# Optimization experiments

Measured on AMD Instinct MI355X. Metric: run time of the kernel, lower is better.

The kernel has to match this reference:

```python
import jax, jax.numpy as jnp
import numpy as np

D_MODEL = 3072
N_HEADS = 24
HEAD_DIM = D_MODEL // N_HEADS          # 128
Q_PROJ = D_MODEL // 2                  # 1536
KV_PROJ = 2 * D_MODEL // 3             # 2048
ROPE_DIM = HEAD_DIM // 2               # 64 (qk_rope_dim == qk_no_rope_dim)
MAX_LEN = 2048
ROPE_THETA = 10000.0
EPS = 1e-6
B, S = 2, 2048


def setup_inputs() -> dict:
    key = jax.random.key(0)
    ks = jax.random.split(key, 7)
    return {
        "x": jax.random.normal(ks[0], (B, S, D_MODEL), dtype=jnp.float32),
        "scale": jnp.ones((D_MODEL,), dtype=jnp.float32),
        "w_dq": 0.01 * jax.random.normal(ks[1], (D_MODEL, Q_PROJ), dtype=jnp.float32),
        "w_uq": 0.01 * jax.random.normal(ks[2], (Q_PROJ, D_MODEL), dtype=jnp.float32),
        "w_dkv": 0.01 * jax.random.normal(ks[3], (D_MODEL, KV_PROJ + ROPE_DIM), dtype=jnp.float32),
        "w_ukv": 0.01 * jax.random.normal(ks[4], (KV_PROJ, D_MODEL + N_HEADS * ROPE_DIM), dtype=jnp.float32),
        "w_o": 0.01 * jax.random.normal(ks[5], (D_MODEL, D_MODEL), dtype=jnp.float32),
    }


def _rope_cos_sin(seq_len):
    # freqs over full head_dim, sliced to rope_dim//2 then tiled x2 (as in torch repeat)
    freqs = 1.0 / (ROPE_THETA ** (jnp.arange(0, HEAD_DIM, 2, dtype=jnp.float32) / HEAD_DIM))
    angles = jnp.arange(seq_len, dtype=jnp.float32)[:, None] * freqs[None, :]  # [S, 64]
    ang = angles[:, : ROPE_DIM // 2]                                            # [S, 32]
    cos = jnp.tile(jnp.cos(ang), (1, 2))                                        # [S, 64]
    sin = jnp.tile(jnp.sin(ang), (1, 2))
    return cos[None, None], sin[None, None]  # [1,1,S,64]


def _rotate_half(t):
    a, b = jnp.split(t, 2, axis=-1)
    return jnp.concatenate([-b, a], axis=-1)


def reference(x, scale, w_dq, w_uq, w_dkv, w_ukv, w_o):
    b, s, _ = x.shape
    # RMSNorm pre-normalization
    xn = scale * (x * jax.lax.rsqrt(jnp.mean(x * x, axis=-1, keepdims=True) + EPS))
    # two-stage query projection
    q = (xn @ w_dq) @ w_uq                                   # [B,S,D]
    q = q.reshape(b, s, N_HEADS, HEAD_DIM).transpose(0, 2, 1, 3)  # [B,H,S,hd]
    q_no_rope, q_rope = jnp.split(q, [ROPE_DIM], axis=-1)
    cos, sin = _rope_cos_sin(s)
    q_rope = q_rope * cos + _rotate_half(q_rope) * sin
    # KV down projection (this is the kv cache)
    kv_down = xn @ w_dkv                                     # [B,S,KV_PROJ+rope]
    kv_no_rope, k_rope = jnp.split(kv_down, [KV_PROJ], axis=-1)
    # KV up projection
    kv_up = kv_no_rope @ w_ukv                               # [B,S,H*(hd+rope)]
    kv_up = kv_up.reshape(b, s, N_HEADS, HEAD_DIM + ROPE_DIM).transpose(0, 2, 1, 3)
    key, value = jnp.split(kv_up, [ROPE_DIM], axis=-1)       # key [B,H,S,64], value [B,H,S,128]
    # shared rope key (one head, broadcast to all heads)
    k_rope = k_rope[:, None, :, :]                           # [B,1,S,64]
    k_rope = k_rope * cos + _rotate_half(k_rope) * sin
    k_rope = jnp.broadcast_to(k_rope, (b, N_HEADS, s, ROPE_DIM))
    final_q = jnp.concatenate([q_no_rope, q_rope], axis=-1)  # [B,H,S,128]
    final_k = jnp.concatenate([key, k_rope], axis=-1)        # [B,H,S,128]
    # masked SDPA (causal, past_length=0)
    inv_scale = 1.0 / jnp.sqrt(jnp.asarray(HEAD_DIM, dtype=x.dtype))
    scores = jnp.einsum("bhsd,bhtd->bhst", final_q, final_k) * inv_scale
    causal = jnp.tril(jnp.ones((s, s), dtype=bool))
    scores = jnp.where(causal[None, None], scores, jnp.asarray(-1e30, dtype=scores.dtype))
    attn = jax.nn.softmax(scores, axis=-1)
    attn_out = jnp.einsum("bhst,bhtd->bhsd", attn, value)    # [B,H,S,128]
    attn_out = attn_out.transpose(0, 2, 1, 3).reshape(b, s, D_MODEL)
    output = attn_out @ w_o.T
    return output, kv_down
```

## Files before the change

### kernel.cpp

```cpp
#include <hip/hip_runtime.h>
#include <hip/hip_bf16.h>
#include <stdint.h>

using bf16_t = __bf16;
using bf16x8 = __attribute__((ext_vector_type(8))) __bf16;
using bf16x4 = __attribute__((ext_vector_type(4))) __bf16;
using f32x4  = __attribute__((ext_vector_type(4))) float;

#define D_MODEL 3072
#define N_HEADS 24
#define HEAD_DIM 128
#define Q_PROJ 1536
#define KV_PROJ 2048
#define ROPE_DIM 64
#define S_LEN 2048
#define NTOK 4096
#define KVDN 2112
#define KVUN 4608

__device__ __forceinline__ void async_ld16(const void* g, void* l) {
    __builtin_amdgcn_global_load_lds(
        (__attribute__((address_space(1))) uint32_t*)(uintptr_t)g,
        (__attribute__((address_space(3))) uint32_t*)(uint32_t)(uintptr_t)l,
        16, 0, 0);
}

#define BARRIER() __builtin_amdgcn_s_barrier()
#define WAITVN(n) asm volatile("s_waitcnt vmcnt(" #n ")" ::: "memory")

__global__ __launch_bounds__(256) void rmsnorm_kernel(
    const float* __restrict__ x, const float* __restrict__ sc, bf16_t* __restrict__ xn)
{
    const int tok = blockIdx.x;
    const int t = threadIdx.x;
    const float4* xr = (const float4*)(x + (size_t)tok * D_MODEL);
    float4 a = xr[t], b = xr[t + 256], c = xr[t + 512];
    float ss = a.x*a.x + a.y*a.y + a.z*a.z + a.w*a.w
             + b.x*b.x + b.y*b.y + b.z*b.z + b.w*b.w
             + c.x*c.x + c.y*c.y + c.z*c.z + c.w*c.w;
    #pragma unroll
    for (int off = 32; off >= 1; off >>= 1) ss += __shfl_xor(ss, off);
    __shared__ float red[4];
    if ((t & 63) == 0) red[t >> 6] = ss;
    __syncthreads();
    const float inv = rsqrtf((red[0] + red[1] + red[2] + red[3]) * (1.0f / D_MODEL) + 1e-6f);
    const float4* sr = (const float4*)sc;
    float4 s0 = sr[t], s1 = sr[t + 256], s2 = sr[t + 512];
    bf16x4* xo = (bf16x4*)(xn + (size_t)tok * D_MODEL);
    bf16x4 o;
    o[0]=(bf16_t)(a.x*s0.x*inv); o[1]=(bf16_t)(a.y*s0.y*inv); o[2]=(bf16_t)(a.z*s0.z*inv); o[3]=(bf16_t)(a.w*s0.w*inv);
    xo[t] = o;
    o[0]=(bf16_t)(b.x*s1.x*inv); o[1]=(bf16_t)(b.y*s1.y*inv); o[2]=(bf16_t)(b.z*s1.z*inv); o[3]=(bf16_t)(b.w*s1.w*inv);
    xo[t + 256] = o;
    o[0]=(bf16_t)(c.x*s2.x*inv); o[1]=(bf16_t)(c.y*s2.y*inv); o[2]=(bf16_t)(c.z*s2.z*inv); o[3]=(bf16_t)(c.w*s2.w*inv);
    xo[t + 512] = o;
}

__global__ __launch_bounds__(256) void prep_weights(
    const float* __restrict__ w_dq, const float* __restrict__ w_uq,
    const float* __restrict__ w_dkv, const float* __restrict__ w_ukv,
    const float* __restrict__ w_o,
    bf16_t* __restrict__ wcat, bf16_t* __restrict__ wuqt,
    bf16_t* __restrict__ wukvt, bf16_t* __restrict__ wob)
{
    __shared__ float tile[32][33];
    int t = blockIdx.x;
    const float* in; bf16_t* out; int K, N, ntx; bool tr = true;
    if (t < 4608)        {            in = w_dq;  out = wcat;                          K = 3072; N = 1536; ntx = 48; }
    else if (t < 10944)  { t -= 4608; in = w_dkv; out = wcat + (size_t)1536 * 3072;    K = 3072; N = 2112; ntx = 66; }
    else if (t < 15552)  { t -= 10944; in = w_uq;  out = wuqt;                         K = 1536; N = 3072; ntx = 96; }
    else if (t < 24768)  { t -= 15552; in = w_ukv; out = wukvt;                        K = 2048; N = 4608; ntx = 144; }
    else                 { t -= 24768; in = w_o;   out = wob;                          K = 3072; N = 3072; ntx = 96; tr = false; }
    const int n0 = (t % ntx) * 32, k0 = (t / ntx) * 32;
    const int tx = threadIdx.x, ty = threadIdx.y;
    if (tr) {
        #pragma unroll
        for (int i = 0; i < 32; i += 8)
            tile[ty + i][tx] = in[(size_t)(k0 + ty + i) * N + n0 + tx];
        __syncthreads();
        #pragma unroll
        for (int i = 0; i < 32; i += 8)
            out[(size_t)(n0 + ty + i) * K + k0 + tx] = (bf16_t)tile[tx][ty + i];
    } else {
        #pragma unroll
        for (int i = 0; i < 32; i += 8)
            out[(size_t)(k0 + ty + i) * N + n0 + tx] =
                (bf16_t)in[(size_t)(k0 + ty + i) * N + n0 + tx];
    }
}

template<int RH, int BNF>
__device__ __forceinline__ void mfmaQ(f32x4 (&acc)[8][BNF], const bf16x8 (&af)[4],
                                      const bf16x8 (&bfv)[BNF]) {
    __builtin_amdgcn_s_setprio(1);
    #pragma unroll
    for (int i = 0; i < 4; ++i)
        #pragma unroll
        for (int cf = 0; cf < BNF; ++cf)
            acc[RH*4+i][cf] = __builtin_amdgcn_mfma_f32_16x16x32_bf16(af[i], bfv[cf], acc[RH*4+i][cf], 0, 0, 0);
    __builtin_amdgcn_s_setprio(0);
}

template<int BNF>
__global__ __launch_bounds__(512, 2) void gemm256(
    const bf16_t* __restrict__ A, const bf16_t* __restrict__ B, int N, int K,
    float* __restrict__ Cf, int ldf, int flo, int fhi,
    bf16_t* __restrict__ Cb1, int ldb1, int b1lo, int b1hi,
    bf16_t* __restrict__ Cb2, int ldb2, int b2lo, int b2hi,
    bf16_t* __restrict__ vt, float cbscale)
{
    constexpr int BN = BNF * 64;
    constexpr uint32_t BSLOT = BNF * 4096;
    __shared__ char LDS[65536 + 4 * BSLOT];
    char* Lc = LDS;
    const int tid = threadIdx.x;
    const int wv = tid >> 6, lane = tid & 63;
    const int fr = lane & 15, fg = lane >> 4;
    const int wr = wv >> 2, wc = wv & 3;
    const bool bwave = (wv < 2 * BNF);

    int lin = blockIdx.y * gridDim.x + blockIdx.x;
    const int nwg = gridDim.x * gridDim.y;
    if ((nwg & 7) == 0) lin = (lin & 7) * (nwg >> 3) + (lin >> 3);
    const int bx = lin % gridDim.x, by = lin / gridDim.x;
    const int m0 = by << 8, n0 = bx * BN;

    const uint32_t slot4 = (uint32_t)((fg ^ ((fr >> 1) & 3)) << 4);

    const bf16_t* agp[2]; const bf16_t* bgp[2];
    uint32_t aoff[2], boff[2];
    #pragma unroll
    for (int j = 0; j < 2; ++j) {
        const int c = j * 512 + tid;
        const int g = c ^ ((c >> 3) & 3);
        agp[j] = A + (size_t)(m0 + (g >> 2)) * K + (g & 3) * 8;
        aoff[j] = (uint32_t)((j * 8 + wv) * 1024);
        const int cb = j * (BNF * 128) + tid;
        const int gb = cb ^ ((cb >> 3) & 3);
        int br = n0 + (gb >> 2); if (br > N - 1) br = N - 1;
        bgp[j] = B + (size_t)br * K + (gb & 3) * 8;
        boff[j] = (uint32_t)(j * (BNF * 2048) + wv * 1024);
    }

    f32x4 acc[8][BNF];
    f32x4 zero = {0.f, 0.f, 0.f, 0.f};
    #pragma unroll
    for (int i = 0; i < 8; ++i)
        #pragma unroll
        for (int j = 0; j < BNF; ++j) acc[i][j] = zero;

    bf16x8 A0[4], A1[4], B0[BNF], B1[BNF];
    const int rowA = (wr << 7) + fr;
    const int rowB = wc * (BNF * 16) + fr;

    auto stA = [&](int t, int kh) {
        const uint32_t sb = (uint32_t)(((2*t + kh) & 3) << 14);
        #pragma unroll
        for (int j = 0; j < 2; ++j)
            async_ld16(agp[j] + t * 64 + kh * 32, Lc + sb + aoff[j]);
    };
    auto stB = [&](int t, int kh) {
        const uint32_t sb = 65536u + (uint32_t)(((2*t + kh) & 3) * BSLOT);
        if (tid < BNF * 128) {
            #pragma unroll
            for (int j = 0; j < 2; ++j)
                async_ld16(bgp[j] + t * 64 + kh * 32, Lc + sb + boff[j]);
        }
    };
    auto ldA4 = [&](int t, int kh, int rh, bf16x8 (&dst)[4]) {
        const uint32_t base = (uint32_t)(((2*t + kh) & 3) << 14);
        #pragma unroll
        for (int i = 0; i < 4; ++i)
            dst[i] = *(const bf16x8*)(Lc + base + (rowA + (rh * 4 + i) * 16) * 64 + slot4);
    };
    auto ldBn = [&](int t, int kh, bf16x8 (&dst)[BNF]) {
        const uint32_t base = 65536u + (uint32_t)(((2*t + kh) & 3) * BSLOT);
        #pragma unroll
        for (int cf = 0; cf < BNF; ++cf)
            dst[cf] = *(const bf16x8*)(Lc + base + (rowB + cf * 16) * 64 + slot4);
    };

    const int NT = K >> 6;
    stA(0, 0); stB(0, 0); stA(0, 1); stB(0, 1);
    stA(1, 0); stB(1, 0); stA(1, 1); stB(1, 1);
    if (bwave) { WAITVN(8); } else { WAITVN(4); }
    BARRIER();
    ldA4(0, 0, 0, A0); ldBn(0, 0, B0);

    for (int t = 0; t < NT; ++t) {
        const bool pref = (t + 2 < NT);
        ldA4(t, 0, 1, A1);
        mfmaQ<0, BNF>(acc, A0, B0);
        if (pref) { if (bwave) { WAITVN(4); } else { WAITVN(2); } }
        else      { WAITVN(0); }
        BARRIER();
        ldA4(t, 1, 0, A0); ldBn(t, 1, B1);
        if (pref) { stA(t + 2, 0); stB(t + 2, 0); }
        mfmaQ<1, BNF>(acc, A1, B0);
        BARRIER();
        ldA4(t, 1, 1, A1);
        mfmaQ<0, BNF>(acc, A0, B1);
        BARRIER();
        if (t + 1 < NT) { ldA4(t + 1, 0, 0, A0); ldBn(t + 1, 0, B0); }
        if (pref) { stA(t + 2, 1); stB(t + 2, 1); }
        mfmaQ<1, BNF>(acc, A1, B1);
        BARRIER();
    }

    const int colb = n0 + wc * (BNF * 16) + fr;
    const int rowb = m0 + (wr << 7) + fg * 4;
    if (vt) {
        #pragma unroll
        for (int rf = 0; rf < 8; ++rf) {
            const int row0 = rowb + rf * 16;
            const int bb = row0 >> 11, s0 = row0 & 2047;
            #pragma unroll
            for (int cf = 0; cf < BNF; ++cf) {
                const int col = colb + cf * 16;
                const int h = col / 192;
                const int dm = col - h * 192;
                if (dm < 64) {
                    #pragma unroll
                    for (int r = 0; r < 4; ++r)
                        Cb1[(size_t)(row0 + r) * ldb1 + col] = (bf16_t)acc[rf][cf][r];
                } else {
                    bf16x4 o;
                    o[0] = (bf16_t)acc[rf][cf][0];
                    o[1] = (bf16_t)acc[rf][cf][1];
                    o[2] = (bf16_t)acc[rf][cf][2];
                    o[3] = (bf16_t)acc[rf][cf][3];
                    *(bf16x4*)(vt + ((size_t)((bb * 24 + h) * 128 + dm - 64)) * 2048 + s0) = o;
                }
            }
        }
    } else {
        #pragma unroll
        for (int rf = 0; rf < 8; ++rf)
            #pragma unroll
            for (int cf = 0; cf < BNF; ++cf) {
                const int col = colb + cf * 16;
                #pragma unroll
                for (int r = 0; r < 4; ++r) {
                    const int row = rowb + rf * 16 + r;
                    const float v = acc[rf][cf][r];
                    if (Cf  && col >= flo  && col < fhi)  Cf [(size_t)row * ldf  + col - flo]  = v;
                    if (Cb1 && col >= b1lo && col < b1hi) Cb1[(size_t)row * ldb1 + col - b1lo] = (bf16_t)(v * cbscale);
                    if (Cb2 && col >= b2lo && col < b2hi) Cb2[(size_t)row * ldb2 + col - b2lo] = (bf16_t)v;
                }
            }
    }
}

__global__ void rope_tab(float* __restrict__ ctab, float* __restrict__ stab)
{
    const int idx = blockIdx.x * 256 + threadIdx.x;
    if (idx >= S_LEN * 32) return;
    const int s = idx >> 5, i = idx & 31;
    const float freq = powf(10000.0f, -(float)(2 * i) * (1.0f / 128.0f));
    const float ang = (float)s * freq;
    ctab[idx] = cosf(ang);
    stab[idx] = sinf(ang);
}

__global__ __launch_bounds__(256) void rope_all(
    bf16_t* __restrict__ q, const float* __restrict__ kvd, bf16_t* __restrict__ kr,
    const float* __restrict__ ctab, const float* __restrict__ stab)
{
    const int idx = blockIdx.x * 256 + threadIdx.x;
    if (idx < NTOK * N_HEADS * 4) {
        const int c = idx & 3;
        const int rest = idx >> 2;
        const int h = rest % N_HEADS;
        const int tok = rest / N_HEADS;
        const int s = tok & (S_LEN - 1);
        bf16_t* p = q + (size_t)tok * D_MODEL + h * HEAD_DIM + 64 + c * 8;
        bf16x8 a = *(const bf16x8*)(p);
        bf16x8 b = *(const bf16x8*)(p + 32);
        const float4* cp = (const float4*)(ctab + s * 32 + c * 8);
        const float4* sp = (const float4*)(stab + s * 32 + c * 8);
        float4 c0 = cp[0], c1 = cp[1];
        float4 s0 = sp[0], s1 = sp[1];
        float cs[8] = {c0.x, c0.y, c0.z, c0.w, c1.x, c1.y, c1.z, c1.w};
        float sn[8] = {s0.x, s0.y, s0.z, s0.w, s1.x, s1.y, s1.z, s1.w};
        bf16x8 oa, ob;
        #pragma unroll
        for (int j = 0; j < 8; ++j) {
            const float av = (float)a[j], bv = (float)b[j];
            oa[j] = (bf16_t)(av * cs[j] - bv * sn[j]);
            ob[j] = (bf16_t)(bv * cs[j] + av * sn[j]);
        }
        *(bf16x8*)(p)      = oa;
        *(bf16x8*)(p + 32) = ob;
    } else {
        const int kx = idx - NTOK * N_HEADS * 4;
        if (kx >= NTOK * 32) return;
        const int i = kx & 31;
        const int tok = kx >> 5;
        const int s = tok & (S_LEN - 1);
        const float* p = kvd + (size_t)tok * KVDN + KV_PROJ;
        const float a = p[i], b = p[i + 32];
        const float c = ctab[s * 32 + i], sn = stab[s * 32 + i];
        kr[(size_t)tok * 64 + i]      = (bf16_t)(a * c - b * sn);
        kr[(size_t)tok * 64 + i + 32] = (bf16_t)(b * c + a * sn);
    }
}

__global__ __launch_bounds__(256, 2) void attn_fwd(
    const bf16_t* __restrict__ Q, const bf16_t* __restrict__ KVUP,
    const bf16_t* __restrict__ KR, const bf16_t* __restrict__ VT,
    bf16_t* __restrict__ AO)
{
    __shared__ bf16_t Knr[2][64 * 64];
    __shared__ bf16_t Krp[2][64 * 64];
    __shared__ bf16_t Vls[2][128 * 64];

    const int bh = blockIdx.y;
    const int b = bh / N_HEADS, h = bh % N_HEADS;
    const int wave = threadIdx.x >> 6, lane = threadIdx.x & 63;
    const int fr = lane & 15, fg = lane >> 4;
    const int rx = fr & 7;
    const int hi = fg >> 1;
    const int s0l = fr + 32 * (fg & 1);
    const int s1l = s0l + 16;

    const bf16_t* Kb  = KVUP + (size_t)b * S_LEN * KVUN + (size_t)h * 192;
    const bf16_t* KRb = KR + (size_t)b * S_LEN * 64;
    const bf16_t* Vb  = VT + (size_t)bh * HEAD_DIM * S_LEN;

    const int srow   = lane >> 3;
    const int schunk = (lane & 7) ^ srow;

    f32x4 zero = {0.f, 0.f, 0.f, 0.f};

    #pragma unroll 1
    for (int tp = 0; tp < 2; ++tp) {
        const int qt = (tp == 0) ? blockIdx.x : (15 - blockIdx.x);
        const int qb = qt * 128;
        const int wrow0 = qb + wave * 32;

        bf16x8 qf[2][4];
        #pragma unroll
        for (int rf = 0; rf < 2; ++rf)
            #pragma unroll
            for (int kc = 0; kc < 4; ++kc)
                qf[rf][kc] = *(const bf16x8*)(Q + (size_t)(b * S_LEN + wrow0 + rf * 16 + fr) * D_MODEL
                                              + h * HEAD_DIM + kc * 32 + fg * 8);
        f32x4 oacc[2][8];
        float m_i[2], l_i[2];
        #pragma unroll
        for (int rf = 0; rf < 2; ++rf) {
            #pragma unroll
            for (int nf = 0; nf < 8; ++nf) oacc[rf][nf] = zero;
            m_i[rf] = -1e30f; l_i[rf] = 0.f;
        }

        auto stage = [&](int kvb, int bf) {
            #pragma unroll
            for (int c = 0; c < 2; ++c) {
                const int r0 = wave * 16 + c * 8;
                async_ld16(Kb  + (size_t)(kvb + r0 + srow) * KVUN + schunk * 8, &Knr[bf][r0 * 64]);
                async_ld16(KRb + (size_t)(kvb + r0 + srow) * 64   + schunk * 8, &Krp[bf][r0 * 64]);
            }
            #pragma unroll
            for (int c = 0; c < 4; ++c) {
                const int r0 = wave * 32 + c * 8;
                async_ld16(Vb + (size_t)(r0 + srow) * S_LEN + kvb + schunk * 8, &Vls[bf][r0 * 64]);
            }
        };

        const int kvend = qb + 128;
        int cur = 0;
        stage(0, 0);
        __syncthreads();

        #pragma unroll 1
        for (int kvb = 0; kvb < kvend; kvb += 64) {
            if (kvb + 64 < kvend) stage(kvb + 64, cur ^ 1);

            if (kvb <= wrow0 + 31) {
                const bf16_t* Kc = Knr[cur];
                const bf16_t* Rc = Krp[cur];
                const bf16_t* Vc = Vls[cur];

                f32x4 sacc[2][4];
                #pragma unroll
                for (int rf = 0; rf < 2; ++rf)
                    #pragma unroll
                    for (int jn = 0; jn < 4; ++jn) sacc[rf][jn] = zero;
                __builtin_amdgcn_s_setprio(1);
                #pragma unroll
                for (int jn = 0; jn < 4; ++jn) {
                    const int krow = jn * 16 + fr;
                    bf16x8 kA = *(const bf16x8*)(Kc + krow * 64 + (((0 + fg) ^ rx) << 3));
                    bf16x8 kB = *(const bf16x8*)(Kc + krow * 64 + (((4 + fg) ^ rx) << 3));
                    bf16x8 kC = *(const bf16x8*)(Rc + krow * 64 + (((0 + fg) ^ rx) << 3));
                    bf16x8 kD = *(const bf16x8*)(Rc + krow * 64 + (((4 + fg) ^ rx) << 3));
                    #pragma unroll
                    for (int rf = 0; rf < 2; ++rf) {
                        sacc[rf][jn] = __builtin_amdgcn_mfma_f32_16x16x32_bf16(kA, qf[rf][0], sacc[rf][jn], 0, 0, 0);
                        sacc[rf][jn] = __builtin_amdgcn_mfma_f32_16x16x32_bf16(kB, qf[rf][1], sacc[rf][jn], 0, 0, 0);
                        sacc[rf][jn] = __builtin_amdgcn_mfma_f32_16x16x32_bf16(kC, qf[rf][2], sacc[rf][jn], 0, 0, 0);
                        sacc[rf][jn] = __builtin_amdgcn_mfma_f32_16x16x32_bf16(kD, qf[rf][3], sacc[rf][jn], 0, 0, 0);
                    }
                }
                __builtin_amdgcn_s_setprio(0);

                const bool needMask = (kvb + 63 > wrow0);
                uint32_t pk[2][4][2];
                #pragma unroll
                for (int rf = 0; rf < 2; ++rf) {
                    const int qrow = wrow0 + rf * 16 + fr;
                    float mx = -1e30f;
                    #pragma unroll
                    for (int jn = 0; jn < 4; ++jn)
                        #pragma unroll
                        for (int r = 0; r < 4; ++r) {
                            float v = sacc[rf][jn][r];
                            if (needMask && (kvb + jn * 16 + fg * 4 + r > qrow)) v = -1e30f;
                            sacc[rf][jn][r] = v;
                            mx = fmaxf(mx, v);
                        }
                    mx = fmaxf(mx, __shfl_xor(mx, 16));
                    mx = fmaxf(mx, __shfl_xor(mx, 32));
                    if (!__all(mx <= m_i[rf] + 8.f)) {
                        const float mn = fmaxf(m_i[rf], mx);
                        const float sc = __builtin_amdgcn_exp2f(m_i[rf] - mn);
                        m_i[rf] = mn;
                        l_i[rf] *= sc;
                        #pragma unroll
                        for (int nf = 0; nf < 8; ++nf)
                            #pragma unroll
                            for (int r = 0; r < 4; ++r) oacc[rf][nf][r] *= sc;
                    }
                    const float mn = m_i[rf];
                    float ls = 0.f;
                    #pragma unroll
                    for (int jn = 0; jn < 4; ++jn) {
                        float p0 = __builtin_amdgcn_exp2f(sacc[rf][jn][0] - mn);
                        float p1 = __builtin_amdgcn_exp2f(sacc[rf][jn][1] - mn);
                        float p2 = __builtin_amdgcn_exp2f(sacc[rf][jn][2] - mn);
                        float p3 = __builtin_amdgcn_exp2f(sacc[rf][jn][3] - mn);
                        ls += (p0 + p1) + (p2 + p3);
                        union { bf16x4 h; uint32_t w[2]; } cv;
                        cv.h[0] = (bf16_t)p0; cv.h[1] = (bf16_t)p1;
                        cv.h[2] = (bf16_t)p2; cv.h[3] = (bf16_t)p3;
                        pk[rf][jn][0] = cv.w[0]; pk[rf][jn][1] = cv.w[1];
                    }
                    ls += __shfl_xor(ls, 16);
                    ls += __shfl_xor(ls, 32);
                    l_i[rf] += ls;
                }

                bf16x8 bfr[2][2];
                #pragma unroll
                for (int rf = 0; rf < 2; ++rf)
                    #pragma unroll
                    for (int ks = 0; ks < 2; ++ks) {
                        const uint32_t t00 = __shfl(pk[rf][2*ks][0],   s0l);
                        const uint32_t t01 = __shfl(pk[rf][2*ks][1],   s0l);
                        const uint32_t t10 = __shfl(pk[rf][2*ks+1][0], s0l);
                        const uint32_t t11 = __shfl(pk[rf][2*ks+1][1], s0l);
                        const uint32_t u00 = __shfl(pk[rf][2*ks][0],   s1l);
                        const uint32_t u01 = __shfl(pk[rf][2*ks][1],   s1l);
                        const uint32_t u10 = __shfl(pk[rf][2*ks+1][0], s1l);
                        const uint32_t u11 = __shfl(pk[rf][2*ks+1][1], s1l);
                        union { bf16x8 h; uint32_t w[4]; } bb;
                        bb.w[0] = hi ? t10 : t00;
                        bb.w[1] = hi ? t11 : t01;
                        bb.w[2] = hi ? u10 : u00;
                        bb.w[3] = hi ? u11 : u01;
                        bfr[rf][ks] = bb.h;
                    }

                __builtin_amdgcn_s_setprio(1);
                #pragma unroll
                for (int nf = 0; nf < 8; ++nf) {
                    const int vrow = nf * 16 + fr;
                    bf16x8 v0 = *(const bf16x8*)(Vc + vrow * 64 + (((0 + fg) ^ rx) << 3));
                    bf16x8 v1 = *(const bf16x8*)(Vc + vrow * 64 + (((4 + fg) ^ rx) << 3));
                    #pragma unroll
                    for (int rf = 0; rf < 2; ++rf) {
                        oacc[rf][nf] = __builtin_amdgcn_mfma_f32_16x16x32_bf16(v0, bfr[rf][0], oacc[rf][nf], 0, 0, 0);
                        oacc[rf][nf] = __builtin_amdgcn_mfma_f32_16x16x32_bf16(v1, bfr[rf][1], oacc[rf][nf], 0, 0, 0);
                    }
                }
                __builtin_amdgcn_s_setprio(0);
            }
            __syncthreads();
            cur ^= 1;
        }

        #pragma unroll
        for (int rf = 0; rf < 2; ++rf) {
            const float rl = __builtin_amdgcn_rcpf(l_i[rf]);
            const int qrow = wrow0 + rf * 16 + fr;
            bf16_t* aob = AO + (size_t)(b * S_LEN + qrow) * D_MODEL + h * HEAD_DIM + fg * 4;
            #pragma unroll
            for (int nf = 0; nf < 8; ++nf) {
                bf16x4 o;
                o[0] = (bf16_t)(oacc[rf][nf][0] * rl);
                o[1] = (bf16_t)(oacc[rf][nf][1] * rl);
                o[2] = (bf16_t)(oacc[rf][nf][2] * rl);
                o[3] = (bf16_t)(oacc[rf][nf][3] * rl);
                *(bf16x4*)(aob + nf * 16) = o;
            }
        }
    }
}

extern "C" void kernel_launch(void* const* d_in, const int* in_sizes, int n_in,
                              void* d_out, int out_size, void* d_ws, size_t ws_size,
                              hipStream_t stream)
{
    const float* x     = (const float*)d_in[0];
    const float* scale = (const float*)d_in[1];
    const float* w_dq  = (const float*)d_in[2];
    const float* w_uq  = (const float*)d_in[3];
    const float* w_dkv = (const float*)d_in[4];
    const float* w_ukv = (const float*)d_in[5];
    const float* w_o   = (const float*)d_in[6];
    float* out0 = (float*)d_out;
    float* out1 = out0 + (size_t)NTOK * D_MODEL;

    if (ws_size < 187039744ull) return;
    char* ws = (char*)d_ws;
    bf16_t* XN    = (bf16_t*)(ws + 0);
    bf16_t* WCAT  = (bf16_t*)(ws + 25165824ull);
    bf16_t* WUQT  = (bf16_t*)(ws + 47579136ull);
    bf16_t* WUKVT = (bf16_t*)(ws + 57016320ull);
    bf16_t* WOB   = (bf16_t*)(ws + 75890688ull);
    bf16_t* QD    = (bf16_t*)(ws + 94765056ull);
    bf16_t* Qb    = (bf16_t*)(ws + 107347968ull);
    bf16_t* KVNR  = (bf16_t*)(ws + 132513792ull);
    bf16_t* KVUP  = (bf16_t*)(ws + 149291008ull);
    bf16_t* KRB   = (bf16_t*)(ws + 94765056ull);
    float*  CTAB  = (float*) (ws + 95289344ull);
    float*  STAB  = (float*) (ws + 95551488ull);
    bf16_t* VTb   = WCAT;
    bf16_t* AO    = XN;

    const float l2e_isc = 0.127500625f;

    rmsnorm_kernel<<<NTOK, 256, 0, stream>>>(x, scale, XN);
    prep_weights<<<33984, dim3(32, 8), 0, stream>>>(w_dq, w_uq, w_dkv, w_ukv, w_o,
                                                    WCAT, WUQT, WUKVT, WOB);

    gemm256<4><<<dim3(15, 16), 512, 0, stream>>>(XN, WCAT, 3648, 3072,
        out1, KVDN, 1536, 3648,
        QD,   Q_PROJ, 0, 1536,
        KVNR, KV_PROJ, 1536, 3584, nullptr, 1.0f);
    gemm256<3><<<dim3(16, 16), 512, 0, stream>>>(QD, WUQT, 3072, 1536,
        nullptr, 0, 0, 0, Qb, D_MODEL, 0, 3072, nullptr, 0, 0, 0, nullptr, l2e_isc);
    rope_tab<<<(S_LEN * 32 + 255) / 256, 256, 0, stream>>>(CTAB, STAB);
    rope_all<<<2048, 256, 0, stream>>>(Qb, out1, KRB, CTAB, STAB);
    gemm256<3><<<dim3(24, 16), 512, 0, stream>>>(KVNR, WUKVT, 4608, 2048,
        nullptr, 0, 0, 0, KVUP, KVUN, 0, 0, nullptr, 0, 0, 0, VTb, 1.0f);
    attn_fwd<<<dim3(8, 48), 256, 0, stream>>>(Qb, KVUP, KRB, VTb, AO);
    gemm256<3><<<dim3(16, 16), 512, 0, stream>>>(AO, WOB, 3072, 3072,
        out0, D_MODEL, 0, 3072, nullptr, 0, 0, 0, nullptr, 0, 0, 0, nullptr, 1.0f);
}
```

Measured before the change: 505.2 us.

## Add 128x192-tile GEMM kernel for up-projection and output GEMMs, vectorize w_o conversion

Adds a gemm128 kernel with 128x192 output tiles, smaller LDS and four blocks per CU, and uses it for the Q up-projection, KV up-projection and output projection. gemm256 keeps only the fused down-projection. Smaller tiles double the grid (256 blocks become 512, 384 become 768), so these GEMMs fill the 256 CUs more evenly and lose less to tail waves. The cost is lower per-tile data reuse and more global traffic. The w_o fp32-to-bf16 copy in prep_weights also moves to a flat float4 path.

```diff
diff --git a/kernel.cpp b/kernel.cpp
--- a/kernel.cpp
+++ b/kernel.cpp
@@ -65,28 +65,29 @@
 {
     __shared__ float tile[32][33];
     int t = blockIdx.x;
-    const float* in; bf16_t* out; int K, N, ntx; bool tr = true;
+    if (t >= 24768) {
+        const int tt = t - 24768;
+        const int idx = tt * 256 + threadIdx.y * 32 + threadIdx.x;
+        float4 v = ((const float4*)w_o)[idx];
+        bf16x4 o;
+        o[0] = (bf16_t)v.x; o[1] = (bf16_t)v.y; o[2] = (bf16_t)v.z; o[3] = (bf16_t)v.w;
+        ((bf16x4*)wob)[idx] = o;
+        return;
+    }
+    const float* in; bf16_t* out; int K, N, ntx;
     if (t < 4608)        {            in = w_dq;  out = wcat;                          K = 3072; N = 1536; ntx = 48; }
     else if (t < 10944)  { t -= 4608; in = w_dkv; out = wcat + (size_t)1536 * 3072;    K = 3072; N = 2112; ntx = 66; }
     else if (t < 15552)  { t -= 10944; in = w_uq;  out = wuqt;                         K = 1536; N = 3072; ntx = 96; }
-    else if (t < 24768)  { t -= 15552; in = w_ukv; out = wukvt;                        K = 2048; N = 4608; ntx = 144; }
-    else                 { t -= 24768; in = w_o;   out = wob;                          K = 3072; N = 3072; ntx = 96; tr = false; }
+    else                 { t -= 15552; in = w_ukv; out = wukvt;                        K = 2048; N = 4608; ntx = 144; }
     const int n0 = (t % ntx) * 32, k0 = (t / ntx) * 32;
     const int tx = threadIdx.x, ty = threadIdx.y;
-    if (tr) {
-        #pragma unroll
-        for (int i = 0; i < 32; i += 8)
-            tile[ty + i][tx] = in[(size_t)(k0 + ty + i) * N + n0 + tx];
-        __syncthreads();
-        #pragma unroll
-        for (int i = 0; i < 32; i += 8)
-            out[(size_t)(n0 + ty + i) * K + k0 + tx] = (bf16_t)tile[tx][ty + i];
-    } else {
-        #pragma unroll
-        for (int i = 0; i < 32; i += 8)
-            out[(size_t)(k0 + ty + i) * N + n0 + tx] =
-                (bf16_t)in[(size_t)(k0 + ty + i) * N + n0 + tx];
-    }
+    #pragma unroll
+    for (int i = 0; i < 32; i += 8)
+        tile[ty + i][tx] = in[(size_t)(k0 + ty + i) * N + n0 + tx];
+    __syncthreads();
+    #pragma unroll
+    for (int i = 0; i < 32; i += 8)
+        out[(size_t)(n0 + ty + i) * K + k0 + tx] = (bf16_t)tile[tx][ty + i];
 }
 
 template<int RH, int BNF>
@@ -106,8 +107,7 @@
     const bf16_t* __restrict__ A, const bf16_t* __restrict__ B, int N, int K,
     float* __restrict__ Cf, int ldf, int flo, int fhi,
     bf16_t* __restrict__ Cb1, int ldb1, int b1lo, int b1hi,
-    bf16_t* __restrict__ Cb2, int ldb2, int b2lo, int b2hi,
-    bf16_t* __restrict__ vt, float cbscale)
+    bf16_t* __restrict__ Cb2, int ldb2, int b2lo, int b2hi)
 {
     constexpr int BN = BNF * 64;
     constexpr uint32_t BSLOT = BNF * 4096;
@@ -209,13 +209,141 @@
 
     const int colb = n0 + wc * (BNF * 16) + fr;
     const int rowb = m0 + (wr << 7) + fg * 4;
+    #pragma unroll
+    for (int rf = 0; rf < 8; ++rf)
+        #pragma unroll
+        for (int cf = 0; cf < BNF; ++cf) {
+            const int col = colb + cf * 16;
+            #pragma unroll
+            for (int r = 0; r < 4; ++r) {
+                const int row = rowb + rf * 16 + r;
+                const float v = acc[rf][cf][r];
+                if (Cf  && col >= flo  && col < fhi)  Cf [(size_t)row * ldf  + col - flo]  = v;
+                if (Cb1 && col >= b1lo && col < b1hi) Cb1[(size_t)row * ldb1 + col - b1lo] = (bf16_t)v;
+                if (Cb2 && col >= b2lo && col < b2hi) Cb2[(size_t)row * ldb2 + col - b2lo] = (bf16_t)v;
+            }
+        }
+}
+
+template<int RH>
+__device__ __forceinline__ void mfmaH(f32x4 (&acc)[4][3], const bf16x8 (&af)[2],
+                                      const bf16x8 (&bfv)[3]) {
+    __builtin_amdgcn_s_setprio(1);
+    #pragma unroll
+    for (int i = 0; i < 2; ++i)
+        #pragma unroll
+        for (int cf = 0; cf < 3; ++cf)
+            acc[RH*2+i][cf] = __builtin_amdgcn_mfma_f32_16x16x32_bf16(af[i], bfv[cf], acc[RH*2+i][cf], 0, 0, 0);
+    __builtin_amdgcn_s_setprio(0);
+}
+
+__global__ __launch_bounds__(512, 4) void gemm128(
+    const bf16_t* __restrict__ A, const bf16_t* __restrict__ B, int N, int K,
+    float* __restrict__ Cf, int ldf,
+    bf16_t* __restrict__ Cb1, int ldb1,
+    bf16_t* __restrict__ vt, float cbscale)
+{
+    __shared__ char LDS[32768 + 49152];
+    char* Lc = LDS;
+    const int tid = threadIdx.x;
+    const int wv = tid >> 6, lane = tid & 63;
+    const int fr = lane & 15, fg = lane >> 4;
+    const int wr = wv >> 2, wc = wv & 3;
+    const bool bwave = (wv < 6);
+
+    int lin = blockIdx.y * gridDim.x + blockIdx.x;
+    const int nwg = gridDim.x * gridDim.y;
+    if ((nwg & 7) == 0) lin = (lin & 7) * (nwg >> 3) + (lin >> 3);
+    const int bx = lin % gridDim.x, by = lin / gridDim.x;
+    const int m0 = by << 7, n0 = bx * 192;
+
+    const uint32_t slot4 = (uint32_t)((fg ^ ((fr >> 1) & 3)) << 4);
+
+    const int ga = tid ^ ((tid >> 3) & 3);
+    const bf16_t* agp = A + (size_t)(m0 + (ga >> 2)) * K + (ga & 3) * 8;
+    const uint32_t aoff = (uint32_t)(wv * 1024);
+    const bf16_t* bgp[2]; uint32_t boff[2];
+    #pragma unroll
+    for (int j = 0; j < 2; ++j) {
+        const int cb = j * 384 + tid;
+        const int gb = cb ^ ((cb >> 3) & 3);
+        int br = n0 + (gb >> 2); if (br > N - 1) br = N - 1;
+        bgp[j] = B + (size_t)br * K + (gb & 3) * 8;
+        boff[j] = (uint32_t)(j * 6144 + wv * 1024);
+    }
+
+    f32x4 acc[4][3];
+    f32x4 zero = {0.f, 0.f, 0.f, 0.f};
+    #pragma unroll
+    for (int i = 0; i < 4; ++i)
+        #pragma unroll
+        for (int j = 0; j < 3; ++j) acc[i][j] = zero;
+
+    bf16x8 A0[2], A1[2], B0[3], B1[3];
+    const int rowA = (wr << 6) + fr;
+    const int rowB = wc * 48 + fr;
+
+    auto stA = [&](int t, int kh) {
+        const uint32_t sb = (uint32_t)(((2*t + kh) & 3) << 13);
+        async_ld16(agp + t * 64 + kh * 32, Lc + sb + aoff);
+    };
+    auto stB = [&](int t, int kh) {
+        const uint32_t sb = 32768u + (uint32_t)(((2*t + kh) & 3) * 12288);
+        if (tid < 384) {
+            #pragma unroll
+            for (int j = 0; j < 2; ++j)
+                async_ld16(bgp[j] + t * 64 + kh * 32, Lc + sb + boff[j]);
+        }
+    };
+    auto ldA2 = [&](int t, int kh, int rh, bf16x8 (&dst)[2]) {
+        const uint32_t base = (uint32_t)(((2*t + kh) & 3) << 13);
+        #pragma unroll
+        for (int i = 0; i < 2; ++i)
+            dst[i] = *(const bf16x8*)(Lc + base + (rowA + (rh * 2 + i) * 16) * 64 + slot4);
+    };
+    auto ldB3 = [&](int t, int kh, bf16x8 (&dst)[3]) {
+        const uint32_t base = 32768u + (uint32_t)(((2*t + kh) & 3) * 12288);
+        #pragma unroll
+        for (int cf = 0; cf < 3; ++cf)
+            dst[cf] = *(const bf16x8*)(Lc + base + (rowB + cf * 16) * 64 + slot4);
+    };
+
+    const int NT = K >> 6;
+    stA(0, 0); stB(0, 0); stA(0, 1); stB(0, 1);
+    stA(1, 0); stB(1, 0); stA(1, 1); stB(1, 1);
+    if (bwave) { WAITVN(6); } else { WAITVN(2); }
+    BARRIER();
+    ldA2(0, 0, 0, A0); ldB3(0, 0, B0);
+
+    for (int t = 0; t < NT; ++t) {
+        const bool pref = (t + 2 < NT);
+        ldA2(t, 0, 1, A1);
+        mfmaH<0>(acc, A0, B0);
+        if (pref) { if (bwave) { WAITVN(3); } else { WAITVN(1); } }
+        else      { WAITVN(0); }
+        BARRIER();
+        ldA2(t, 1, 0, A0); ldB3(t, 1, B1);
+        if (pref) { stA(t + 2, 0); stB(t + 2, 0); }
+        mfmaH<1>(acc, A1, B0);
+        BARRIER();
+        ldA2(t, 1, 1, A1);
+        mfmaH<0>(acc, A0, B1);
+        BARRIER();
+        if (t + 1 < NT) { ldA2(t + 1, 0, 0, A0); ldB3(t + 1, 0, B0); }
+        if (pref) { stA(t + 2, 1); stB(t + 2, 1); }
+        mfmaH<1>(acc, A1, B1);
+        BARRIER();
+    }
+
+    const int colb = n0 + wc * 48 + fr;
+    const int rowb = m0 + (wr << 6) + fg * 4;
     if (vt) {
         #pragma unroll
-        for (int rf = 0; rf < 8; ++rf) {
+        for (int rf = 0; rf < 4; ++rf) {
             const int row0 = rowb + rf * 16;
             const int bb = row0 >> 11, s0 = row0 & 2047;
             #pragma unroll
-            for (int cf = 0; cf < BNF; ++cf) {
+            for (int cf = 0; cf < 3; ++cf) {
                 const int col = colb + cf * 16;
                 const int h = col / 192;
                 const int dm = col - h * 192;
@@ -235,17 +363,16 @@
         }
     } else {
         #pragma unroll
-        for (int rf = 0; rf < 8; ++rf)
-            #pragma unroll
-            for (int cf = 0; cf < BNF; ++cf) {
+        for (int rf = 0; rf < 4; ++rf)
+            #pragma unroll
+            for (int cf = 0; cf < 3; ++cf) {
                 const int col = colb + cf * 16;
                 #pragma unroll
                 for (int r = 0; r < 4; ++r) {
                     const int row = rowb + rf * 16 + r;
                     const float v = acc[rf][cf][r];
-                    if (Cf  && col >= flo  && col < fhi)  Cf [(size_t)row * ldf  + col - flo]  = v;
-                    if (Cb1 && col >= b1lo && col < b1hi) Cb1[(size_t)row * ldb1 + col - b1lo] = (bf16_t)(v * cbscale);
-                    if (Cb2 && col >= b2lo && col < b2hi) Cb2[(size_t)row * ldb2 + col - b2lo] = (bf16_t)v;
+                    if (Cf)  Cf [(size_t)row * ldf  + col] = v;
+                    if (Cb1) Cb1[(size_t)row * ldb1 + col] = (bf16_t)(v * cbscale);
                 }
             }
     }
@@ -548,14 +675,14 @@
     gemm256<4><<<dim3(15, 16), 512, 0, stream>>>(XN, WCAT, 3648, 3072,
         out1, KVDN, 1536, 3648,
         QD,   Q_PROJ, 0, 1536,
-        KVNR, KV_PROJ, 1536, 3584, nullptr, 1.0f);
-    gemm256<3><<<dim3(16, 16), 512, 0, stream>>>(QD, WUQT, 3072, 1536,
-        nullptr, 0, 0, 0, Qb, D_MODEL, 0, 3072, nullptr, 0, 0, 0, nullptr, l2e_isc);
+        KVNR, KV_PROJ, 1536, 3584);
+    gemm128<<<dim3(16, 32), 512, 0, stream>>>(QD, WUQT, 3072, 1536,
+        nullptr, 0, Qb, D_MODEL, nullptr, l2e_isc);
     rope_tab<<<(S_LEN * 32 + 255) / 256, 256, 0, stream>>>(CTAB, STAB);
     rope_all<<<2048, 256, 0, stream>>>(Qb, out1, KRB, CTAB, STAB);
-    gemm256<3><<<dim3(24, 16), 512, 0, stream>>>(KVNR, WUKVT, 4608, 2048,
-        nullptr, 0, 0, 0, KVUP, KVUN, 0, 0, nullptr, 0, 0, 0, VTb, 1.0f);
+    gemm128<<<dim3(24, 32), 512, 0, stream>>>(KVNR, WUKVT, 4608, 2048,
+        nullptr, 0, KVUP, KVUN, VTb, 1.0f);
     attn_fwd<<<dim3(8, 48), 256, 0, stream>>>(Qb, KVUP, KRB, VTb, AO);
-    gemm256<3><<<dim3(16, 16), 512, 0, stream>>>(AO, WOB, 3072, 3072,
-        out0, D_MODEL, 0, 3072, nullptr, 0, 0, 0, nullptr, 0, 0, 0, nullptr, 1.0f);
-}
+    gemm128<<<dim3(16, 32), 512, 0, stream>>>(AO, WOB, 3072, 3072,
+        out0, D_MODEL, nullptr, 0, nullptr, 1.0f);
+}
```

Result: no change. 500.6 us, median of 2 (-0.9%).

## Shrink GEMM tiles to 128x192 with higher occupancy; vectorize w_o cast

Applied to the files above, without the earlier changes.

Replaces the templated 256-row GEMM with a fixed 128x192 tile kernel that uses half the A staging and smaller accumulators, and launches with a min-4-blocks occupancy bound. All four projection GEMMs now launch twice as many workgroups, which spreads better across CUs. The untransposed w_o conversion is also split out into a float4-vectorized path. Smaller tiles give less operand reuse per MFMA, so global and LDS traffic per flop goes up.

```diff
diff --git a/kernel.cpp b/kernel.cpp
--- a/kernel.cpp
+++ b/kernel.cpp
@@ -65,157 +65,151 @@
 {
     __shared__ float tile[32][33];
     int t = blockIdx.x;
-    const float* in; bf16_t* out; int K, N, ntx; bool tr = true;
+    if (t >= 24768) {
+        const int tt = t - 24768;
+        const int idx = tt * 256 + threadIdx.y * 32 + threadIdx.x;
+        float4 v = ((const float4*)w_o)[idx];
+        bf16x4 o;
+        o[0] = (bf16_t)v.x; o[1] = (bf16_t)v.y; o[2] = (bf16_t)v.z; o[3] = (bf16_t)v.w;
+        ((bf16x4*)wob)[idx] = o;
+        return;
+    }
+    const float* in; bf16_t* out; int K, N, ntx;
     if (t < 4608)        {            in = w_dq;  out = wcat;                          K = 3072; N = 1536; ntx = 48; }
     else if (t < 10944)  { t -= 4608; in = w_dkv; out = wcat + (size_t)1536 * 3072;    K = 3072; N = 2112; ntx = 66; }
     else if (t < 15552)  { t -= 10944; in = w_uq;  out = wuqt;                         K = 1536; N = 3072; ntx = 96; }
-    else if (t < 24768)  { t -= 15552; in = w_ukv; out = wukvt;                        K = 2048; N = 4608; ntx = 144; }
-    else                 { t -= 24768; in = w_o;   out = wob;                          K = 3072; N = 3072; ntx = 96; tr = false; }
+    else                 { t -= 15552; in = w_ukv; out = wukvt;                        K = 2048; N = 4608; ntx = 144; }
     const int n0 = (t % ntx) * 32, k0 = (t / ntx) * 32;
     const int tx = threadIdx.x, ty = threadIdx.y;
-    if (tr) {
-        #pragma unroll
-        for (int i = 0; i < 32; i += 8)
-            tile[ty + i][tx] = in[(size_t)(k0 + ty + i) * N + n0 + tx];
-        __syncthreads();
-        #pragma unroll
-        for (int i = 0; i < 32; i += 8)
-            out[(size_t)(n0 + ty + i) * K + k0 + tx] = (bf16_t)tile[tx][ty + i];
-    } else {
-        #pragma unroll
-        for (int i = 0; i < 32; i += 8)
-            out[(size_t)(k0 + ty + i) * N + n0 + tx] =
-                (bf16_t)in[(size_t)(k0 + ty + i) * N + n0 + tx];
-    }
-}
-
-template<int RH, int BNF>
-__device__ __forceinline__ void mfmaQ(f32x4 (&acc)[8][BNF], const bf16x8 (&af)[4],
-                                      const bf16x8 (&bfv)[BNF]) {
+    #pragma unroll
+    for (int i = 0; i < 32; i += 8)
+        tile[ty + i][tx] = in[(size_t)(k0 + ty + i) * N + n0 + tx];
+    __syncthreads();
+    #pragma unroll
+    for (int i = 0; i < 32; i += 8)
+        out[(size_t)(n0 + ty + i) * K + k0 + tx] = (bf16_t)tile[tx][ty + i];
+}
+
+template<int RH>
+__device__ __forceinline__ void mfmaH(f32x4 (&acc)[4][3], const bf16x8 (&af)[2],
+                                      const bf16x8 (&bfv)[3]) {
     __builtin_amdgcn_s_setprio(1);
     #pragma unroll
-    for (int i = 0; i < 4; ++i)
-        #pragma unroll
-        for (int cf = 0; cf < BNF; ++cf)
-            acc[RH*4+i][cf] = __builtin_amdgcn_mfma_f32_16x16x32_bf16(af[i], bfv[cf], acc[RH*4+i][cf], 0, 0, 0);
+    for (int i = 0; i < 2; ++i)
+        #pragma unroll
+        for (int cf = 0; cf < 3; ++cf)
+            acc[RH*2+i][cf] = __builtin_amdgcn_mfma_f32_16x16x32_bf16(af[i], bfv[cf], acc[RH*2+i][cf], 0, 0, 0);
     __builtin_amdgcn_s_setprio(0);
 }
 
-template<int BNF>
-__global__ __launch_bounds__(512, 2) void gemm256(
+__global__ __launch_bounds__(512, 4) void gemm128(
     const bf16_t* __restrict__ A, const bf16_t* __restrict__ B, int N, int K,
     float* __restrict__ Cf, int ldf, int flo, int fhi,
     bf16_t* __restrict__ Cb1, int ldb1, int b1lo, int b1hi,
     bf16_t* __restrict__ Cb2, int ldb2, int b2lo, int b2hi,
     bf16_t* __restrict__ vt, float cbscale)
 {
-    constexpr int BN = BNF * 64;
-    constexpr uint32_t BSLOT = BNF * 4096;
-    __shared__ char LDS[65536 + 4 * BSLOT];
+    __shared__ char LDS[32768 + 49152];
     char* Lc = LDS;
     const int tid = threadIdx.x;
     const int wv = tid >> 6, lane = tid & 63;
     const int fr = lane & 15, fg = lane >> 4;
     const int wr = wv >> 2, wc = wv & 3;
-    const bool bwave = (wv < 2 * BNF);
+    const bool bwave = (wv < 6);
 
     int lin = blockIdx.y * gridDim.x + blockIdx.x;
     const int nwg = gridDim.x * gridDim.y;
     if ((nwg & 7) == 0) lin = (lin & 7) * (nwg >> 3) + (lin >> 3);
     const int bx = lin % gridDim.x, by = lin / gridDim.x;
-    const int m0 = by << 8, n0 = bx * BN;
+    const int m0 = by << 7, n0 = bx * 192;
 
     const uint32_t slot4 = (uint32_t)((fg ^ ((fr >> 1) & 3)) << 4);
 
-    const bf16_t* agp[2]; const bf16_t* bgp[2];
-    uint32_t aoff[2], boff[2];
+    const int ga = tid ^ ((tid >> 3) & 3);
+    const bf16_t* agp = A + (size_t)(m0 + (ga >> 2)) * K + (ga & 3) * 8;
+    const uint32_t aoff = (uint32_t)(wv * 1024);
+    const bf16_t* bgp[2]; uint32_t boff[2];
     #pragma unroll
     for (int j = 0; j < 2; ++j) {
-        const int c = j * 512 + tid;
-        const int g = c ^ ((c >> 3) & 3);
-        agp[j] = A + (size_t)(m0 + (g >> 2)) * K + (g & 3) * 8;
-        aoff[j] = (uint32_t)((j * 8 + wv) * 1024);
-        const int cb = j * (BNF * 128) + tid;
+        const int cb = j * 384 + tid;
         const int gb = cb ^ ((cb >> 3) & 3);
         int br = n0 + (gb >> 2); if (br > N - 1) br = N - 1;
         bgp[j] = B + (size_t)br * K + (gb & 3) * 8;
-        boff[j] = (uint32_t)(j * (BNF * 2048) + wv * 1024);
+        boff[j] = (uint32_t)(j * 6144 + wv * 1024);
     }
 
-    f32x4 acc[8][BNF];
+    f32x4 acc[4][3];
     f32x4 zero = {0.f, 0.f, 0.f, 0.f};
     #pragma unroll
-    for (int i = 0; i < 8; ++i)
-        #pragma unroll
-        for (int j = 0; j < BNF; ++j) acc[i][j] = zero;
-
-    bf16x8 A0[4], A1[4], B0[BNF], B1[BNF];
-    const int rowA = (wr << 7) + fr;
-    const int rowB = wc * (BNF * 16) + fr;
+    for (int i = 0; i < 4; ++i)
+        #pragma unroll
+        for (int j = 0; j < 3; ++j) acc[i][j] = zero;
+
+    bf16x8 A0[2], A1[2], B0[3], B1[3];
+    const int rowA = (wr << 6) + fr;
+    const int rowB = wc * 48 + fr;
 
     auto stA = [&](int t, int kh) {
-        const uint32_t sb = (uint32_t)(((2*t + kh) & 3) << 14);
-        #pragma unroll
-        for (int j = 0; j < 2; ++j)
-            async_ld16(agp[j] + t * 64 + kh * 32, Lc + sb + aoff[j]);
+        const uint32_t sb = (uint32_t)(((2*t + kh) & 3) << 13);
+        async_ld16(agp + t * 64 + kh * 32, Lc + sb + aoff);
     };
     auto stB = [&](int t, int kh) {
-        const uint32_t sb = 65536u + (uint32_t)(((2*t + kh) & 3) * BSLOT);
-        if (tid < BNF * 128) {
+        const uint32_t sb = 32768u + (uint32_t)(((2*t + kh) & 3) * 12288);
+        if (tid < 384) {
             #pragma unroll
             for (int j = 0; j < 2; ++j)
                 async_ld16(bgp[j] + t * 64 + kh * 32, Lc + sb + boff[j]);
         }
     };
-    auto ldA4 = [&](int t, int kh, int rh, bf16x8 (&dst)[4]) {
-        const uint32_t base = (uint32_t)(((2*t + kh) & 3) << 14);
-        #pragma unroll
-        for (int i = 0; i < 4; ++i)
-            dst[i] = *(const bf16x8*)(Lc + base + (rowA + (rh * 4 + i) * 16) * 64 + slot4);
+    auto ldA2 = [&](int t, int kh, int rh, bf16x8 (&dst)[2]) {
+        const uint32_t base = (uint32_t)(((2*t + kh) & 3) << 13);
+        #pragma unroll
+        for (int i = 0; i < 2; ++i)
+            dst[i] = *(const bf16x8*)(Lc + base + (rowA + (rh * 2 + i) * 16) * 64 + slot4);
     };
-    auto ldBn = [&](int t, int kh, bf16x8 (&dst)[BNF]) {
-        const uint32_t base = 65536u + (uint32_t)(((2*t + kh) & 3) * BSLOT);
-        #pragma unroll
-        for (int cf = 0; cf < BNF; ++cf)
+    auto ldB3 = [&](int t, int kh, bf16x8 (&dst)[3]) {
+        const uint32_t base = 32768u + (uint32_t)(((2*t + kh) & 3) * 12288);
+        #pragma unroll
+        for (int cf = 0; cf < 3; ++cf)
             dst[cf] = *(const bf16x8*)(Lc + base + (rowB + cf * 16) * 64 + slot4);
     };
 
     const int NT = K >> 6;
     stA(0, 0); stB(0, 0); stA(0, 1); stB(0, 1);
     stA(1, 0); stB(1, 0); stA(1, 1); stB(1, 1);
-    if (bwave) { WAITVN(8); } else { WAITVN(4); }
+    if (bwave) { WAITVN(6); } else { WAITVN(2); }
     BARRIER();
-    ldA4(0, 0, 0, A0); ldBn(0, 0, B0);
+    ldA2(0, 0, 0, A0); ldB3(0, 0, B0);
 
     for (int t = 0; t < NT; ++t) {
         const bool pref = (t + 2 < NT);
-        ldA4(t, 0, 1, A1);
-        mfmaQ<0, BNF>(acc, A0, B0);
-        if (pref) { if (bwave) { WAITVN(4); } else { WAITVN(2); } }
+        ldA2(t, 0, 1, A1);
+        mfmaH<0>(acc, A0, B0);
+        if (pref) { if (bwave) { WAITVN(3); } else { WAITVN(1); } }
         else      { WAITVN(0); }
         BARRIER();
-        ldA4(t, 1, 0, A0); ldBn(t, 1, B1);
+        ldA2(t, 1, 0, A0); ldB3(t, 1, B1);
         if (pref) { stA(t + 2, 0); stB(t + 2, 0); }
-        mfmaQ<1, BNF>(acc, A1, B0);
+        mfmaH<1>(acc, A1, B0);
         BARRIER();
-        ldA4(t, 1, 1, A1);
-        mfmaQ<0, BNF>(acc, A0, B1);
+        ldA2(t, 1, 1, A1);
+        mfmaH<0>(acc, A0, B1);
         BARRIER();
-        if (t + 1 < NT) { ldA4(t + 1, 0, 0, A0); ldBn(t + 1, 0, B0); }
+        if (t + 1 < NT) { ldA2(t + 1, 0, 0, A0); ldB3(t + 1, 0, B0); }
         if (pref) { stA(t + 2, 1); stB(t + 2, 1); }
-        mfmaQ<1, BNF>(acc, A1, B1);
+        mfmaH<1>(acc, A1, B1);
         BARRIER();
     }
 
-    const int colb = n0 + wc * (BNF * 16) + fr;
-    const int rowb = m0 + (wr << 7) + fg * 4;
+    const int colb = n0 + wc * 48 + fr;
+    const int rowb = m0 + (wr << 6) + fg * 4;
     if (vt) {
         #pragma unroll
-        for (int rf = 0; rf < 8; ++rf) {
+        for (int rf = 0; rf < 4; ++rf) {
             const int row0 = rowb + rf * 16;
             const int bb = row0 >> 11, s0 = row0 & 2047;
             #pragma unroll
-            for (int cf = 0; cf < BNF; ++cf) {
+            for (int cf = 0; cf < 3; ++cf) {
                 const int col = colb + cf * 16;
                 const int h = col / 192;
                 const int dm = col - h * 192;
@@ -235,9 +229,9 @@
         }
     } else {
         #pragma unroll
-        for (int rf = 0; rf < 8; ++rf)
-            #pragma unroll
-            for (int cf = 0; cf < BNF; ++cf) {
+        for (int rf = 0; rf < 4; ++rf)
+            #pragma unroll
+            for (int cf = 0; cf < 3; ++cf) {
                 const int col = colb + cf * 16;
                 #pragma unroll
                 for (int r = 0; r < 4; ++r) {
@@ -545,17 +539,17 @@
     prep_weights<<<33984, dim3(32, 8), 0, stream>>>(w_dq, w_uq, w_dkv, w_ukv, w_o,
                                                     WCAT, WUQT, WUKVT, WOB);
 
-    gemm256<4><<<dim3(15, 16), 512, 0, stream>>>(XN, WCAT, 3648, 3072,
+    gemm128<<<dim3(19, 32), 512, 0, stream>>>(XN, WCAT, 3648, 3072,
         out1, KVDN, 1536, 3648,
         QD,   Q_PROJ, 0, 1536,
         KVNR, KV_PROJ, 1536, 3584, nullptr, 1.0f);
-    gemm256<3><<<dim3(16, 16), 512, 0, stream>>>(QD, WUQT, 3072, 1536,
+    gemm128<<<dim3(16, 32), 512, 0, stream>>>(QD, WUQT, 3072, 1536,
         nullptr, 0, 0, 0, Qb, D_MODEL, 0, 3072, nullptr, 0, 0, 0, nullptr, l2e_isc);
     rope_tab<<<(S_LEN * 32 + 255) / 256, 256, 0, stream>>>(CTAB, STAB);
     rope_all<<<2048, 256, 0, stream>>>(Qb, out1, KRB, CTAB, STAB);
-    gemm256<3><<<dim3(24, 16), 512, 0, stream>>>(KVNR, WUKVT, 4608, 2048,
+    gemm128<<<dim3(24, 32), 512, 0, stream>>>(KVNR, WUKVT, 4608, 2048,
         nullptr, 0, 0, 0, KVUP, KVUN, 0, 0, nullptr, 0, 0, 0, VTb, 1.0f);
     attn_fwd<<<dim3(8, 48), 256, 0, stream>>>(Qb, KVUP, KRB, VTb, AO);
-    gemm256<3><<<dim3(16, 16), 512, 0, stream>>>(AO, WOB, 3072, 3072,
+    gemm128<<<dim3(16, 32), 512, 0, stream>>>(AO, WOB, 3072, 3072,
         out0, D_MODEL, 0, 3072, nullptr, 0, 0, 0, nullptr, 0, 0, 0, nullptr, 1.0f);
 }
```

Measured after the change: 534.2 us. 1.06x slower.
